# Performance work log

Hardware: AMD Instinct MI355X
Metric: run time of the kernel (lower is better)

The kernel has to match this reference:

```python
import jax, jax.numpy as jnp
import numpy as np

DIM = 2048; H = 16; QLR = 512; KVLR = 512
NOPE = 128; ROPE = 64; VHD = 128
QKHD = NOPE + ROPE
SCALE = QKHD ** -0.5
EPS = 1.1920929e-07  # torch RMSNorm default eps = finfo(float32).eps
B = 1; S = 2048

def _rmsnorm(x, w):
    return x * jax.lax.rsqrt(jnp.mean(x * x, axis=-1, keepdims=True) + EPS) * w

def _rope(x, cos, sin):
    # x: [b, s, h, d]; cos/sin: [s, d//2] (consecutive-pair complex rotation)
    b, s, h, d = x.shape
    x2 = x.reshape(b, s, h, d // 2, 2)
    x0, x1 = x2[..., 0], x2[..., 1]
    c = cos[None, :, None, :]; sn = sin[None, :, None, :]
    y = jnp.stack([x0 * c - x1 * sn, x0 * sn + x1 * c], axis=-1)
    return y.reshape(b, s, h, d)

def setup_inputs() -> dict:
    key = jax.random.key(0)
    ks = jax.random.split(key, 12)
    def lin(k, fan_in, fan_out):
        bound = 1.0 / np.sqrt(fan_in)
        kw, kb = jax.random.split(k)
        w = jax.random.uniform(kw, (fan_out, fan_in), jnp.float32, -bound, bound)
        b = jax.random.uniform(kb, (fan_out,), jnp.float32, -bound, bound)
        return w, b
    x = jax.random.normal(ks[0], (B, S, DIM), jnp.float32)
    theta = jax.random.uniform(ks[1], (S, ROPE // 2), jnp.float32, 0.0, 2 * np.pi)
    freqs_cos = jnp.cos(theta); freqs_sin = jnp.sin(theta)
    mask = jnp.where(jnp.triu(jnp.ones((S, S), bool), k=1), jnp.float32(-1e9), jnp.float32(0.0))
    wq_a_w, wq_a_b = lin(ks[2], DIM, QLR)
    q_norm_w = jnp.ones((QLR,), jnp.float32)
    wq_b_w, wq_b_b = lin(ks[3], QLR, H * QKHD)
    wkv_a_w, wkv_a_b = lin(ks[4], DIM, KVLR + ROPE)
    kv_norm_w = jnp.ones((KVLR,), jnp.float32)
    wkv_b_w, wkv_b_b = lin(ks[5], KVLR, H * (NOPE + VHD))
    wo_w, wo_b = lin(ks[6], H * VHD, DIM)
    return {"x": x, "start_pos": 0, "freqs_cos": freqs_cos, "freqs_sin": freqs_sin,
            "mask": mask, "wq_a_w": wq_a_w, "wq_a_b": wq_a_b, "q_norm_w": q_norm_w,
            "wq_b_w": wq_b_w, "wq_b_b": wq_b_b, "wkv_a_w": wkv_a_w, "wkv_a_b": wkv_a_b,
            "kv_norm_w": kv_norm_w, "wkv_b_w": wkv_b_w, "wkv_b_b": wkv_b_b,
            "wo_w": wo_w, "wo_b": wo_b}

def reference(x, start_pos, freqs_cos, freqs_sin, mask,
              wq_a_w, wq_a_b, q_norm_w, wq_b_w, wq_b_b,
              wkv_a_w, wkv_a_b, kv_norm_w, wkv_b_w, wkv_b_b, wo_w, wo_b):
    bsz, seqlen, _ = x.shape
    # low-rank query: wq_b(q_norm(wq_a(x)))
    q = _rmsnorm(x @ wq_a_w.T + wq_a_b, q_norm_w) @ wq_b_w.T + wq_b_b
    q = q.reshape(bsz, seqlen, H, QKHD)
    q_nope, q_pe = q[..., :NOPE], q[..., NOPE:]
    q_pe = _rope(q_pe, freqs_cos, freqs_sin)
    kv = x @ wkv_a_w.T + wkv_a_b
    kv_lat, k_pe = kv[..., :KVLR], kv[..., KVLR:]
    k_pe = _rope(k_pe[:, :, None, :], freqs_cos, freqs_sin)  # [b,s,1,ROPE]
    q = jnp.concatenate([q_nope, q_pe], axis=-1)
    kvb = (_rmsnorm(kv_lat, kv_norm_w) @ wkv_b_w.T + wkv_b_b).reshape(bsz, seqlen, H, NOPE + VHD)
    k_nope, v = kvb[..., :NOPE], kvb[..., NOPE:]
    k = jnp.concatenate([k_nope, jnp.broadcast_to(k_pe, (bsz, seqlen, H, ROPE))], axis=-1)
    # prefill (start_pos=0): cache[:end_pos] == freshly written k/v
    scores = jnp.einsum('bshd,bthd->bsht', q, k) * SCALE
    scores = scores + mask[None, :, None, :]
    probs = jax.nn.softmax(scores.astype(jnp.float32), axis=-1).astype(x.dtype)
    out = jnp.einsum('bsht,bthd->bshd', probs, v).reshape(bsz, seqlen, H * VHD)
    return out @ wo_w.T + wo_b
```

## Files before the change

### kernel.cpp

```cpp
#include <hip/hip_runtime.h>
#include <hip/hip_bf16.h>

typedef __attribute__((ext_vector_type(8))) short short8x;
typedef __attribute__((ext_vector_type(4))) short short4x;
typedef __attribute__((ext_vector_type(4))) float float4x;
typedef __hip_bfloat16 bf16;

#define EPS_F 1.1920929e-07f
#define SCALE_F 0.07216878364870323f

__device__ inline float rdv(const void* p, size_t i, int f32) {
  return f32 ? ((const float*)p)[i] : __bfloat162float(((const bf16*)p)[i]);
}

__device__ inline int4 pack8(const float* s) {
  unsigned short h[8];
#pragma unroll
  for (int t = 0; t < 8; t++) {
    bf16 b = __float2bfloat16(s[t]);
    __builtin_memcpy(&h[t], &b, 2);
  }
  int4 r;
  r.x = (int)((unsigned)h[0] | ((unsigned)h[1] << 16));
  r.y = (int)((unsigned)h[2] | ((unsigned)h[3] << 16));
  r.z = (int)((unsigned)h[4] | ((unsigned)h[5] << 16));
  r.w = (int)((unsigned)h[6] | ((unsigned)h[7] << 16));
  return r;
}

typedef __attribute__((address_space(1))) const unsigned int gu32;
typedef __attribute__((address_space(3))) unsigned int lu32;
__device__ __forceinline__ void gload16(const void* g, void* l) {
  __builtin_amdgcn_global_load_lds((gu32*)g, (lu32*)l, 16, 0, 0);
}

__device__ __forceinline__ int detect_exponents(const unsigned short* __restrict__ x,
                                                int tid, int* red) {
  int cnt = 0;
#pragma unroll
  for (int i = 0; i < 4; i++) {
    unsigned short u = x[tid * 4 + i];
    int e = (u >> 7) & 0xFF;
    cnt += (e >= 118 && e <= 130) ? 1 : 0;
  }
#pragma unroll
  for (int off = 1; off < 64; off <<= 1) cnt += __shfl_xor(cnt, off);
  if ((tid & 63) == 0) red[tid >> 6] = cnt;
  __syncthreads();
  return ((red[0] + red[1] + red[2] + red[3]) > 768) ? 0 : 1;
}

__global__ __launch_bounds__(256) void detect_dtype(const unsigned short* __restrict__ x,
                                                    int* __restrict__ flag) {
  __shared__ int red[4];
  int f = detect_exponents(x, threadIdx.x, red);
  if (threadIdx.x == 0) flag[0] = f;
}

__global__ __launch_bounds__(256) void sentinel_kernel(bf16* out, int n) {
  int i = blockIdx.x * 256 + threadIdx.x;
  if (i < n) out[i] = __float2bfloat16(1000.0f);
}

__device__ __forceinline__ void cvt8(const void* src, bf16* dst, size_t i, int f32) {
  if (f32) {
    float4 a = *(const float4*)((const float*)src + i);
    float4 b = *(const float4*)((const float*)src + i + 4);
    float s[8] = {a.x, a.y, a.z, a.w, b.x, b.y, b.z, b.w};
    *(int4*)(dst + i) = pack8(s);
  } else {
    *(int4*)(dst + i) = *(const int4*)((const bf16*)src + i);
  }
}

__global__ __launch_bounds__(256) void convert_in1(
    const void* __restrict__ x, const void* __restrict__ wqa,
    const void* __restrict__ wkva,
    const void* __restrict__ qab, const void* __restrict__ kvab,
    bf16* __restrict__ xb, bf16* __restrict__ wqab, bf16* __restrict__ wkvab,
    bf16* __restrict__ qabb, bf16* __restrict__ kvabb,
    const int* __restrict__ flagp)
{
  const int f32 = flagp[0];
  const int b = blockIdx.x, tid = threadIdx.x;
  if (b < 2048)       { size_t i = ((size_t)b * 256 + tid) * 8;          cvt8(x,    xb,    i, f32); }
  else if (b < 2560)  { size_t i = ((size_t)(b - 2048) * 256 + tid) * 8; cvt8(wqa,  wqab,  i, f32); }
  else if (b < 3136)  { size_t i = ((size_t)(b - 2560) * 256 + tid) * 8; cvt8(wkva, wkvab, i, f32); }
  else {
    for (int i = tid; i < 512; i += 256) qabb[i]  = __float2bfloat16(rdv(qab,  i, f32));
    for (int i = tid; i < 576; i += 256) kvabb[i] = __float2bfloat16(rdv(kvab, i, f32));
  }
}

__global__ __launch_bounds__(256) void convert_in2(
    const void* __restrict__ wqb, const void* __restrict__ wkvb,
    const void* __restrict__ qbb, const void* __restrict__ kvbb,
    bf16* __restrict__ wqbb, bf16* __restrict__ wkvbb,
    bf16* __restrict__ qbbb, bf16* __restrict__ kvbbb,
    const int* __restrict__ flagp)
{
  const int f32 = flagp[0];
  const int b = blockIdx.x, tid = threadIdx.x;
  if (b < 768)        { size_t i = ((size_t)b * 256 + tid) * 8;          cvt8(wqb,  wqbb,  i, f32); }
  else if (b < 1792)  { size_t i = ((size_t)(b - 768) * 256 + tid) * 8;  cvt8(wkvb, wkvbb, i, f32); }
  else if (b == 1792) { for (int i = tid; i < 3072; i += 256) qbbb[i]  = __float2bfloat16(rdv(qbb,  i, f32)); }
  else                { for (int i = tid; i < 4096; i += 256) kvbbb[i] = __float2bfloat16(rdv(kvbb, i, f32)); }
}

__global__ __launch_bounds__(256) void convert_wo(
    const void* __restrict__ wo, const void* __restrict__ wob_in,
    bf16* __restrict__ wo16, bf16* __restrict__ wob16,
    const int* __restrict__ flagp)
{
  const int f32 = flagp[0];
  const int b = blockIdx.x, tid = threadIdx.x;
  if (b < 2048) { size_t i = ((size_t)b * 256 + tid) * 8; cvt8(wo, wo16, i, f32); }
  else { for (int i = tid; i < 2048; i += 256) wob16[i] = __float2bfloat16(rdv(wob_in, i, f32)); }
}

__global__ __launch_bounds__(256) void convert_all(
    const void* __restrict__ x,
    const void* __restrict__ wqa, const void* __restrict__ wkva,
    const void* __restrict__ qab, const void* __restrict__ kvab,
    const void* __restrict__ wqb, const void* __restrict__ wkvb,
    const void* __restrict__ qbb, const void* __restrict__ kvbb,
    const void* __restrict__ wo, const void* __restrict__ wob_in,
    bf16* __restrict__ xb, bf16* __restrict__ wqab, bf16* __restrict__ wkvab,
    bf16* __restrict__ qabb, bf16* __restrict__ kvabb,
    bf16* __restrict__ wqbb, bf16* __restrict__ wkvbb,
    bf16* __restrict__ qbbb, bf16* __restrict__ kvbbb,
    bf16* __restrict__ wo16, bf16* __restrict__ wob16,
    int* __restrict__ flag)
{
  __shared__ int red[4];
  const int b = blockIdx.x, tid = threadIdx.x;
  const int f32 = detect_exponents((const unsigned short*)x, tid, red);
  if (b < 2048)       { size_t i = ((size_t)b * 256 + tid) * 8;          cvt8(x,    xb,    i, f32); }
  else if (b < 2560)  { size_t i = ((size_t)(b - 2048) * 256 + tid) * 8; cvt8(wqa,  wqab,  i, f32); }
  else if (b < 3136)  { size_t i = ((size_t)(b - 2560) * 256 + tid) * 8; cvt8(wkva, wkvab, i, f32); }
  else if (b == 3136) {
    for (int i = tid; i < 512; i += 256) qabb[i]  = __float2bfloat16(rdv(qab,  i, f32));
    for (int i = tid; i < 576; i += 256) kvabb[i] = __float2bfloat16(rdv(kvab, i, f32));
    if (tid == 0) flag[0] = f32;
  }
  else if (b < 5185)  { size_t i = ((size_t)(b - 3137) * 256 + tid) * 8; cvt8(wo, wo16, i, f32); }
  else if (b == 5185) { for (int i = tid; i < 2048; i += 256) wob16[i] = __float2bfloat16(rdv(wob_in, i, f32)); }
  else if (b < 5954)  { size_t i = ((size_t)(b - 5186) * 256 + tid) * 8; cvt8(wqb,  wqbb,  i, f32); }
  else if (b < 6978)  { size_t i = ((size_t)(b - 5954) * 256 + tid) * 8; cvt8(wkvb, wkvbb, i, f32); }
  else if (b == 6978) { for (int i = tid; i < 3072; i += 256) qbbb[i]  = __float2bfloat16(rdv(qbb,  i, f32)); }
  else                { for (int i = tid; i < 4096; i += 256) kvbbb[i] = __float2bfloat16(rdv(kvbb, i, f32)); }
}

template<int OMODE, bool A_DYN>
__device__ __forceinline__ void gemm128_body(
    const void* __restrict__ A, const void* __restrict__ W,
    const void* __restrict__ bias, void* __restrict__ Cout,
    int M, int N, int K, int f32in, int bx, int by,
    int kbeg, int kend, int addbias)
{
  __shared__ int4 As4[128 * 4];
  __shared__ int4 Bs4[128 * 4];
  const int tid = threadIdx.x, lane = tid & 63, wave = tid >> 6;
  const int grp = lane >> 4, l16 = lane & 15;
  const int m0 = bx * 128, n0 = by * 128;
  const int wm = (wave & 1) * 64, wn = (wave >> 1) * 64;
  float4x acc[4][4] = {};
  for (int k0 = kbeg; k0 < kend; k0 += 32) {
    if (!f32in) {
#pragma unroll
      for (int j = 0; j < 2; j++) {
        int row = wave * 32 + j * 16 + (lane >> 2);
        int cs = (lane & 3) ^ ((row >> 1) & 3);
        gload16((const bf16*)A + (size_t)(m0 + row) * K + k0 + cs * 8,
                &As4[(wave * 32 + j * 16) * 4]);
        gload16((const bf16*)W + (size_t)(n0 + row) * K + k0 + cs * 8,
                &Bs4[(wave * 32 + j * 16) * 4]);
      }
    } else {
#pragma unroll
      for (int i = 0; i < 2; i++) {
        int ch = tid + i * 256;
        int row = ch >> 2, c = ch & 3;
        int cs = c ^ ((row >> 1) & 3);
        size_t aoff = (size_t)(m0 + row) * K + k0 + cs * 8;
        size_t boff = (size_t)(n0 + row) * K + k0 + cs * 8;
        As4[row * 4 + c] = A_DYN ? pack8((const float*)A + aoff)
                                 : *(const int4*)((const bf16*)A + aoff);
        Bs4[row * 4 + c] = pack8((const float*)W + boff);
      }
    }
    __syncthreads();
    short8x af[4], bfr[4];
#pragma unroll
    for (int i = 0; i < 4; i++) {
      int ra = wm + i * 16 + l16;
      int rb = wn + i * 16 + l16;
      af[i]  = *(const short8x*)&As4[ra * 4 + (grp ^ ((ra >> 1) & 3))];
      bfr[i] = *(const short8x*)&Bs4[rb * 4 + (grp ^ ((rb >> 1) & 3))];
    }
#pragma unroll
    for (int i = 0; i < 4; i++)
#pragma unroll
      for (int j = 0; j < 4; j++)
        acc[i][j] = __builtin_amdgcn_mfma_f32_16x16x32_bf16(af[i], bfr[j], acc[i][j], 0, 0, 0);
    __syncthreads();
  }
#pragma unroll
  for (int j = 0; j < 4; j++) {
    int gn = n0 + wn + j * 16 + l16;
    float bv = addbias ? rdv(bias, gn, f32in) : 0.0f;
#pragma unroll
    for (int i = 0; i < 4; i++) {
      int gm0 = m0 + wm + i * 16 + grp * 4;
#pragma unroll
      for (int r = 0; r < 4; r++) {
        float v = acc[i][j][r] + bv;
        size_t idx = (size_t)(gm0 + r) * N + gn;
        if (OMODE == 0)      ((float*)Cout)[idx] = v;
        else if (OMODE == 1) ((bf16*)Cout)[idx] = __float2bfloat16(v);
        else {
          if (f32in) ((float*)Cout)[idx] = v;
          else       ((bf16*)Cout)[idx] = __float2bfloat16(v);
        }
      }
    }
  }
}

__global__ __launch_bounds__(256) void gemmB_dual(
    const void* __restrict__ A0, const void* __restrict__ A1,
    const void* __restrict__ W0, const void* __restrict__ W1,
    const void* __restrict__ b0, const void* __restrict__ b1,
    void* __restrict__ C0, void* __restrict__ C1)
{
  const int z = blockIdx.z;
  if (z == 0 && blockIdx.y >= 24) return;
  const void* A = z ? A1 : A0;
  const void* W = z ? W1 : W0;
  const void* bias = z ? b1 : b0;
  void* C = z ? C1 : C0;
  const int N = z ? 4096 : 3072;
  gemm128_body<1, false>(A, W, bias, C, 2048, N, 512, 0,
                         blockIdx.x, blockIdx.y, 0, 512, 1);
}

__global__ __launch_bounds__(256) void gemmWo_sk(
    const void* __restrict__ A, const void* __restrict__ W,
    const void* __restrict__ bias, float* __restrict__ part,
    const int* __restrict__ flagp)
{
  const int z = blockIdx.z;
  gemm128_body<0, false>(A, W, bias, part + (size_t)z * 2048 * 2048,
                         2048, 2048, 2048, flagp[0],
                         blockIdx.x, blockIdx.y, z * 1024, z * 1024 + 1024, z == 0);
}

__global__ __launch_bounds__(256) void gemmWo_sk_bf(
    const void* __restrict__ A, const void* __restrict__ W,
    const void* __restrict__ bias, float* __restrict__ part)
{
  const int z = blockIdx.z;
  gemm128_body<0, false>(A, W, bias, part + (size_t)z * 2048 * 2048,
                         2048, 2048, 2048, 0,
                         blockIdx.x, blockIdx.y, z * 1024, z * 1024 + 1024, z == 0);
}

__global__ __launch_bounds__(256) void reduce_out(
    const float* __restrict__ p0, const float* __restrict__ p1,
    void* __restrict__ out, const int* __restrict__ flagp)
{
  const int f32in = flagp[0];
  size_t i = ((size_t)blockIdx.x * 256 + threadIdx.x) * 4;
  float4 a = *(const float4*)(p0 + i);
  float4 b = *(const float4*)(p1 + i);
  a.x += b.x; a.y += b.y; a.z += b.z; a.w += b.w;
  if (f32in) {
    *(float4*)((float*)out + i) = a;
  } else {
    unsigned short h[4];
    bf16 t0 = __float2bfloat16(a.x); __builtin_memcpy(&h[0], &t0, 2);
    bf16 t1 = __float2bfloat16(a.y); __builtin_memcpy(&h[1], &t1, 2);
    bf16 t2 = __float2bfloat16(a.z); __builtin_memcpy(&h[2], &t2, 2);
    bf16 t3 = __float2bfloat16(a.w); __builtin_memcpy(&h[3], &t3, 2);
    int2 v;
    v.x = (int)((unsigned)h[0] | ((unsigned)h[1] << 16));
    v.y = (int)((unsigned)h[2] | ((unsigned)h[3] << 16));
    *(int2*)((bf16*)out + i) = v;
  }
}

template<int OMODE, bool A_DYN>
__device__ __forceinline__ void gemm64_body(
    const void* __restrict__ A, const void* __restrict__ W,
    const void* __restrict__ bias, void* __restrict__ Cout,
    int M, int N, int K, int f32in, int bx, int by,
    int kbeg, int kend, int addbias)
{
  __shared__ int4 As4[64 * 4];
  __shared__ int4 Bs4[64 * 4];
  const int tid = threadIdx.x, lane = tid & 63, wave = tid >> 6;
  const int grp = lane >> 4, l16 = lane & 15;
  const int m0 = bx * 64, n0 = by * 64;
  const int wm = (wave & 1) * 32, wn = (wave >> 1) * 32;
  float4x acc[2][2] = {};
  for (int k0 = kbeg; k0 < kend; k0 += 32) {
    if (!f32in) {
      int row = wave * 16 + (lane >> 2);
      int cs = (lane & 3) ^ ((row >> 1) & 3);
      gload16((const bf16*)A + (size_t)(m0 + row) * K + k0 + cs * 8,
              &As4[wave * 16 * 4]);
      gload16((const bf16*)W + (size_t)(n0 + row) * K + k0 + cs * 8,
              &Bs4[wave * 16 * 4]);
    } else {
      int row = tid >> 2, c = tid & 3;
      int cs = c ^ ((row >> 1) & 3);
      size_t aoff = (size_t)(m0 + row) * K + k0 + cs * 8;
      size_t boff = (size_t)(n0 + row) * K + k0 + cs * 8;
      As4[row * 4 + c] = A_DYN ? pack8((const float*)A + aoff)
                               : *(const int4*)((const bf16*)A + aoff);
      Bs4[row * 4 + c] = pack8((const float*)W + boff);
    }
    __syncthreads();
    short8x af[2], bfr[2];
#pragma unroll
    for (int i = 0; i < 2; i++) {
      int ra = wm + i * 16 + l16;
      int rb = wn + i * 16 + l16;
      af[i]  = *(const short8x*)&As4[ra * 4 + (grp ^ ((ra >> 1) & 3))];
      bfr[i] = *(const short8x*)&Bs4[rb * 4 + (grp ^ ((rb >> 1) & 3))];
    }
#pragma unroll
    for (int i = 0; i < 2; i++)
#pragma unroll
      for (int j = 0; j < 2; j++)
        acc[i][j] = __builtin_amdgcn_mfma_f32_16x16x32_bf16(af[i], bfr[j], acc[i][j], 0, 0, 0);
    __syncthreads();
  }
#pragma unroll
  for (int j = 0; j < 2; j++) {
    int gn = n0 + wn + j * 16 + l16;
    float bv = addbias ? rdv(bias, gn, f32in) : 0.0f;
#pragma unroll
    for (int i = 0; i < 2; i++) {
      int gm0 = m0 + wm + i * 16 + grp * 4;
#pragma unroll
      for (int r = 0; r < 4; r++) {
        float v = acc[i][j][r] + bv;
        size_t idx = (size_t)(gm0 + r) * N + gn;
        if (OMODE == 0)      ((float*)Cout)[idx] = v;
        else if (OMODE == 1) ((bf16*)Cout)[idx] = __float2bfloat16(v);
        else {
          if (f32in) ((float*)Cout)[idx] = v;
          else       ((bf16*)Cout)[idx] = __float2bfloat16(v);
        }
      }
    }
  }
}

__global__ __launch_bounds__(256) void gemmA_sk(
    const void* __restrict__ A,
    const void* __restrict__ W0, const void* __restrict__ W1,
    const void* __restrict__ b0, const void* __restrict__ b1,
    float* __restrict__ C0, float* __restrict__ C1)
{
  const int z = blockIdx.z;
  const int mat = z >> 1, kh = z & 1;
  const int N = mat ? 576 : 512;
  if (blockIdx.y * 64 >= N) return;
  const void* W = mat ? W1 : W0;
  const void* bias = mat ? b1 : b0;
  float* C = (mat ? C1 : C0) + (size_t)kh * 2048 * N;
  gemm64_body<0, false>(A, W, bias, C, 2048, N, 2048, 0,
                        blockIdx.x, blockIdx.y,
                        kh * 1024, kh * 1024 + 1024, kh == 0);
}

__global__ __launch_bounds__(256) void norms_merged(
    const float* __restrict__ q_a0, const float* __restrict__ q_a1,
    const float* __restrict__ kv_a0, const float* __restrict__ kv_a1,
    const void* __restrict__ qw, const void* __restrict__ kvw,
    const void* __restrict__ cosb, const void* __restrict__ sinb,
    bf16* __restrict__ qn, bf16* __restrict__ kvn, bf16* __restrict__ kpe,
    const int* __restrict__ flagp)
{
  const int f32in = flagp[0];
  const int b = blockIdx.x, tid = threadIdx.x;
  __shared__ float red[4];
  if (b < 2048) {
    const int s = b;
    size_t base = (size_t)s * 512;
    float v0 = q_a0[base + tid] + q_a1[base + tid];
    float v1 = q_a0[base + tid + 256] + q_a1[base + tid + 256];
    float ss = v0 * v0 + v1 * v1;
#pragma unroll
    for (int off = 1; off < 64; off <<= 1) ss += __shfl_xor(ss, off);
    if ((tid & 63) == 0) red[tid >> 6] = ss;
    __syncthreads();
    float tot = red[0] + red[1] + red[2] + red[3];
    float scale = rsqrtf(tot * (1.0f / 512.0f) + EPS_F);
    qn[base + tid]       = __float2bfloat16(v0 * scale * rdv(qw, tid, f32in));
    qn[base + tid + 256] = __float2bfloat16(v1 * scale * rdv(qw, tid + 256, f32in));
  } else {
    const int s = b - 2048;
    size_t base = (size_t)s * 576;
    float v0 = kv_a0[base + tid] + kv_a1[base + tid];
    float v1 = kv_a0[base + tid + 256] + kv_a1[base + tid + 256];
    float ss = v0 * v0 + v1 * v1;
#pragma unroll
    for (int off = 1; off < 64; off <<= 1) ss += __shfl_xor(ss, off);
    if ((tid & 63) == 0) red[tid >> 6] = ss;
    __syncthreads();
    float tot = red[0] + red[1] + red[2] + red[3];
    float scale = rsqrtf(tot * (1.0f / 512.0f) + EPS_F);
    kvn[(size_t)s * 512 + tid]       = __float2bfloat16(v0 * scale * rdv(kvw, tid, f32in));
    kvn[(size_t)s * 512 + tid + 256] = __float2bfloat16(v1 * scale * rdv(kvw, tid + 256, f32in));
    if (tid < 32) {
      float x0 = kv_a0[base + 512 + 2 * tid] + kv_a1[base + 512 + 2 * tid];
      float x1 = kv_a0[base + 512 + 2 * tid + 1] + kv_a1[base + 512 + 2 * tid + 1];
      float c  = rdv(cosb, (size_t)s * 32 + tid, f32in);
      float sn = rdv(sinb, (size_t)s * 32 + tid, f32in);
      kpe[s * 64 + 2 * tid]     = __float2bfloat16(x0 * c - x1 * sn);
      kpe[s * 64 + 2 * tid + 1] = __float2bfloat16(x0 * sn + x1 * c);
    }
  }
}

__global__ __launch_bounds__(256) void rope_vt_merged(
    bf16* __restrict__ q, const void* __restrict__ cosb,
    const void* __restrict__ sinb, const bf16* __restrict__ kvb,
    bf16* __restrict__ Vt, const int* __restrict__ flagp)
{
  const int b = blockIdx.x, tid = threadIdx.x;
  __shared__ __align__(16) bf16 tile[64][136];
  if (b < 2048) {
    const int f32in = flagp[0];
    const int s = b;
#pragma unroll
    for (int it = 0; it < 2; it++) {
      int p = tid + it * 256;
      int hh = p >> 5, jj = p & 31;
      bf16* src = q + (size_t)s * 3072 + hh * 192 + 128 + 2 * jj;
      float x0 = __bfloat162float(src[0]);
      float x1 = __bfloat162float(src[1]);
      float c  = rdv(cosb, (size_t)s * 32 + jj, f32in);
      float sn = rdv(sinb, (size_t)s * 32 + jj, f32in);
      src[0] = __float2bfloat16(x0 * c - x1 * sn);
      src[1] = __float2bfloat16(x0 * sn + x1 * c);
    }
  } else {
    const int hb = b - 2048;
    const int h = hb & 15;
    const int t0 = (hb >> 4) * 64;
#pragma unroll
    for (int i = 0; i < 4; i++) {
      int chunk = tid + i * 256;
      int row = chunk >> 4;
      int c8 = (chunk & 15) * 8;
      *(int4*)&tile[row][c8] =
          *(const int4*)(kvb + (size_t)(t0 + row) * 4096 + h * 256 + 128 + c8);
    }
    __syncthreads();
#pragma unroll
    for (int i = 0; i < 32; i++) {
      int idx = tid + i * 256;
      int d = idx >> 6;
      int t = idx & 63;
      Vt[((size_t)h * 128 + d) * 2048 + t0 + t] = tile[t][d];
    }
  }
}

__global__ __launch_bounds__(256) void attn_kernel(
    const bf16* __restrict__ Q, const bf16* __restrict__ kvb,
    const bf16* __restrict__ kpe, const bf16* __restrict__ Vt,
    bf16* __restrict__ Out)
{
  __shared__ __align__(16) bf16 Ks[64 * 200];
  __shared__ __align__(16) bf16 Vs[128 * 72];
  __shared__ __align__(16) bf16 plds[4][16 * 68];
  const int b = blockIdx.x;
  const int h = b & 15;
  const int tt = (b >> 4) & 15;
  const int q0 = ((b >> 8) ? (31 - tt) : tt) * 64;
  const int tid = threadIdx.x;
  const int wave = tid >> 6;
  const int lane = tid & 63;
  const int grp = lane >> 4, l16 = lane & 15;
  const int qrt = q0 + wave * 16;
  const bf16* Qbase = Q + (size_t)(qrt + l16) * 3072 + h * 192;
  short8x qf[6];
#pragma unroll
  for (int c = 0; c < 6; c++)
    qf[c] = *(const short8x*)(Qbase + c * 32 + grp * 8);
  float m_run[4], l_run[4];
  float4x o_acc[8] = {};
#pragma unroll
  for (int r = 0; r < 4; r++) { m_run[r] = -__builtin_inff(); l_run[r] = 0.f; }
  bf16* pl = &plds[wave][0];
  for (int t0 = 0; t0 <= q0; t0 += 64) {
#pragma unroll
    for (int i = 0; i < 4; i++) {
      int ch = tid + i * 256;
      int row = ch >> 4, c = ch & 15;
      *(int4*)&Ks[row * 200 + c * 8] =
          *(const int4*)(kvb + (size_t)(t0 + row) * 4096 + h * 256 + c * 8);
    }
#pragma unroll
    for (int i = 0; i < 2; i++) {
      int ch = tid + i * 256;
      int row = ch >> 3, c = ch & 7;
      *(int4*)&Ks[row * 200 + 128 + c * 8] =
          *(const int4*)(kpe + (size_t)(t0 + row) * 64 + c * 8);
    }
#pragma unroll
    for (int i = 0; i < 4; i++) {
      int ch = tid + i * 256;
      int row = ch >> 3, c = ch & 7;
      *(int4*)&Vs[row * 72 + c * 8] =
          *(const int4*)(Vt + ((size_t)h * 128 + row) * 2048 + t0 + c * 8);
    }
    __syncthreads();
    float4x sacc[4] = {};
#pragma unroll
    for (int n = 0; n < 4; n++) {
      const bf16* Kb = &Ks[(n * 16 + l16) * 200 + grp * 8];
#pragma unroll
      for (int c = 0; c < 6; c++) {
        short8x kf = *(const short8x*)(Kb + c * 32);
        sacc[n] = __builtin_amdgcn_mfma_f32_16x16x32_bf16(qf[c], kf, sacc[n], 0, 0, 0);
      }
    }
    float pv[4][4], alpha[4];
#pragma unroll
    for (int r = 0; r < 4; r++) {
      const int s_row = qrt + grp * 4 + r;
      float p0[4];
      float mx = -__builtin_inff();
#pragma unroll
      for (int n = 0; n < 4; n++) {
        int t = t0 + n * 16 + l16;
        float v = sacc[n][r] * SCALE_F;
        v = (t > s_row) ? -1.0e9f : v;
        p0[n] = v;
        mx = fmaxf(mx, v);
      }
      mx = fmaxf(mx, __shfl_xor(mx, 1));
      mx = fmaxf(mx, __shfl_xor(mx, 2));
      mx = fmaxf(mx, __shfl_xor(mx, 4));
      mx = fmaxf(mx, __shfl_xor(mx, 8));
      float m_new = fmaxf(m_run[r], mx);
      float a = __expf(m_run[r] - m_new);
      m_run[r] = m_new;
      float sum = 0.f;
#pragma unroll
      for (int n = 0; n < 4; n++) {
        float e = __expf(p0[n] - m_new);
        pv[n][r] = e;
        sum += e;
      }
      sum += __shfl_xor(sum, 1);
      sum += __shfl_xor(sum, 2);
      sum += __shfl_xor(sum, 4);
      sum += __shfl_xor(sum, 8);
      l_run[r] = l_run[r] * a + sum;
      alpha[r] = a;
    }
#pragma unroll
    for (int n = 0; n < 8; n++)
#pragma unroll
      for (int r = 0; r < 4; r++)
        o_acc[n][r] *= alpha[r];
#pragma unroll
    for (int n = 0; n < 4; n++)
#pragma unroll
      for (int r = 0; r < 4; r++)
        pl[(grp * 4 + r) * 68 + n * 16 + l16] = __float2bfloat16(pv[n][r]);
#pragma unroll
    for (int c = 0; c < 2; c++) {
      union { short4x h4[2]; short8x v8; } pk;
      const bf16* pp = pl + l16 * 68 + c * 32 + grp * 8;
      pk.h4[0] = *(const short4x*)(pp);
      pk.h4[1] = *(const short4x*)(pp + 4);
#pragma unroll
      for (int n = 0; n < 8; n++) {
        short8x vf = *(const short8x*)&Vs[(size_t)(n * 16 + l16) * 72 + c * 32 + grp * 8];
        o_acc[n] = __builtin_amdgcn_mfma_f32_16x16x32_bf16(pk.v8, vf, o_acc[n], 0, 0, 0);
      }
    }
    __syncthreads();
  }
  float inv[4];
#pragma unroll
  for (int r = 0; r < 4; r++) inv[r] = 1.0f / l_run[r];
#pragma unroll
  for (int n = 0; n < 8; n++)
#pragma unroll
    for (int r = 0; r < 4; r++) {
      int s_row = qrt + grp * 4 + r;
      Out[(size_t)s_row * 2048 + h * 128 + n * 16 + l16] =
          __float2bfloat16(o_acc[n][r] * inv[r]);
    }
}

extern "C" void kernel_launch(void* const* d_in, const int* in_sizes, int n_in,
                              void* d_out, int out_size, void* d_ws, size_t ws_size,
                              hipStream_t stream) {
  const void* x        = d_in[0];
  const void* fcos     = d_in[2];
  const void* fsin     = d_in[3];
  const void* wq_a_w   = d_in[5];
  const void* wq_a_b   = d_in[6];
  const void* q_norm_w = d_in[7];
  const void* wq_b_w   = d_in[8];
  const void* wq_b_b   = d_in[9];
  const void* wkv_a_w  = d_in[10];
  const void* wkv_a_b  = d_in[11];
  const void* kv_norm_w= d_in[12];
  const void* wkv_b_w  = d_in[13];
  const void* wkv_b_b  = d_in[14];
  const void* wo_w     = d_in[15];
  const void* wo_b     = d_in[16];

  const size_t KB = 1024, MB = 1024 * 1024;
  if (ws_size < 46 * MB) {
    sentinel_kernel<<<(out_size + 255) / 256, 256, 0, stream>>>((bf16*)d_out, out_size);
    return;
  }
  char* ws = (char*)d_ws;
  bf16*  kpe    = (bf16*)(ws);
  int*   flag   = (int*)(ws + 256 * KB);
  bf16*  qbuf   = (bf16*)(ws + 512 * KB);
  bf16*  kvb    = (bf16*)(ws + 12 * MB + 512 * KB);
  bf16*  Vt     = (bf16*)(ws + 28 * MB + 512 * KB);
  bf16*  attnout= (bf16*)(ws + 36 * MB + 512 * KB);
  float* kv_a0  = (float*)(ws + 512 * KB);
  float* kv_a1  = (float*)(ws + 5 * MB);
  float* q_a0   = (float*)(ws + 36 * MB + 512 * KB);
  float* q_a1   = (float*)(ws + 40 * MB + 512 * KB);
  bf16*  qn     = (bf16*)(ws + 28 * MB + 512 * KB);
  bf16*  kvn    = (bf16*)(ws + 30 * MB + 512 * KB);
  float* wpart  = (float*)(ws + 512 * KB);
  bf16*  xb     = (bf16*)(ws + 12 * MB + 512 * KB);
  bf16*  wqab   = (bf16*)(ws + 20 * MB + 512 * KB);
  bf16*  wkvab  = (bf16*)(ws + 22 * MB + 512 * KB);
  bf16*  qabb   = (bf16*)(ws + 25 * MB);
  bf16*  kvabb  = (bf16*)(ws + 25 * MB + 64 * KB);
  bf16*  wqbb_m = (bf16*)(ws + 36 * MB + 512 * KB);
  bf16*  wkvbb_m= (bf16*)(ws + 39 * MB + 512 * KB);
  bf16*  qbbb_m = (bf16*)(ws + 43 * MB + 512 * KB);
  bf16*  kvbbb_m= (bf16*)(ws + 43 * MB + 768 * KB);
  bf16*  wo16   = (bf16*)(ws + 46 * MB);
  bf16*  wob16  = (bf16*)(ws + 54 * MB + 512 * KB);
  bf16*  wqbb_b = (bf16*)(ws + 56 * MB);
  bf16*  wkvbb_b= (bf16*)(ws + 59 * MB);
  bf16*  qbbb_b = (bf16*)(ws + 63 * MB);
  bf16*  kvbbb_b= (bf16*)(ws + 63 * MB + 64 * KB);

  const bool wofast = (ws_size >= 56 * MB);
  const bool bigws  = (ws_size >= 64 * MB);

  dim3 blk(256);
  if (bigws) {
    convert_all<<<6980, blk, 0, stream>>>(
        x, wq_a_w, wkv_a_w, wq_a_b, wkv_a_b, wq_b_w, wkv_b_w, wq_b_b, wkv_b_b,
        wo_w, wo_b,
        xb, wqab, wkvab, qabb, kvabb, wqbb_b, wkvbb_b, qbbb_b, kvbbb_b,
        wo16, wob16, flag);
    gemmA_sk<<<dim3(32, 9, 4), blk, 0, stream>>>(
        xb, wqab, wkvab, qabb, kvabb, q_a0, kv_a0);
    norms_merged<<<4096, blk, 0, stream>>>(
        q_a0, q_a1, kv_a0, kv_a1, q_norm_w, kv_norm_w, fcos, fsin,
        qn, kvn, kpe, flag);
    gemmB_dual<<<dim3(16, 32, 2), blk, 0, stream>>>(
        qn, kvn, wqbb_b, wkvbb_b, qbbb_b, kvbbb_b, qbuf, kvb);
    rope_vt_merged<<<2560, blk, 0, stream>>>(qbuf, fcos, fsin, kvb, Vt, flag);
    attn_kernel<<<dim3(512), blk, 0, stream>>>(qbuf, kvb, kpe, Vt, attnout);
    gemmWo_sk_bf<<<dim3(16, 16, 2), blk, 0, stream>>>(attnout, wo16, wob16, wpart);
    reduce_out<<<4096, blk, 0, stream>>>(wpart, wpart + (size_t)2048 * 2048, d_out, flag);
  } else {
    detect_dtype<<<1, blk, 0, stream>>>((const unsigned short*)x, flag);
    convert_in1<<<3137, blk, 0, stream>>>(
        x, wq_a_w, wkv_a_w, wq_a_b, wkv_a_b, xb, wqab, wkvab, qabb, kvabb, flag);
    if (wofast)
      convert_wo<<<2049, blk, 0, stream>>>(wo_w, wo_b, wo16, wob16, flag);
    gemmA_sk<<<dim3(32, 9, 4), blk, 0, stream>>>(
        xb, wqab, wkvab, qabb, kvabb, q_a0, kv_a0);
    norms_merged<<<4096, blk, 0, stream>>>(
        q_a0, q_a1, kv_a0, kv_a1, q_norm_w, kv_norm_w, fcos, fsin,
        qn, kvn, kpe, flag);
    convert_in2<<<1794, blk, 0, stream>>>(
        wq_b_w, wkv_b_w, wq_b_b, wkv_b_b, wqbb_m, wkvbb_m, qbbb_m, kvbbb_m, flag);
    gemmB_dual<<<dim3(16, 32, 2), blk, 0, stream>>>(
        qn, kvn, wqbb_m, wkvbb_m, qbbb_m, kvbbb_m, qbuf, kvb);
    rope_vt_merged<<<2560, blk, 0, stream>>>(qbuf, fcos, fsin, kvb, Vt, flag);
    attn_kernel<<<dim3(512), blk, 0, stream>>>(qbuf, kvb, kpe, Vt, attnout);
    if (wofast)
      gemmWo_sk_bf<<<dim3(16, 16, 2), blk, 0, stream>>>(attnout, wo16, wob16, wpart);
    else
      gemmWo_sk<<<dim3(16, 16, 2), blk, 0, stream>>>(attnout, wo_w, wo_b, wpart, flag);
    reduce_out<<<4096, blk, 0, stream>>>(wpart, wpart + (size_t)2048 * 2048, d_out, flag);
  }
}
```

Baseline: 315.3 us.

## Fuse q RoPE and V transpose into the second-stage projection GEMM epilogue

Adds a gemmB_fused kernel that applies rotary embedding to the q_pe columns and writes V in transposed layout straight from the GEMM accumulators. This removes the separate rope_vt_merged pass and its extra global read/write of qbuf and kvb. It is gated on the workspace being at least 68 MB and uses new qn4/kvn4 buffers. The epilogue adds cross-lane shuffles, per-element cos/sin loads and scattered stores, and the K loop loads tiles without double buffering.

```diff
diff --git a/kernel.cpp b/kernel.cpp
--- a/kernel.cpp
+++ b/kernel.cpp
@@ -242,6 +242,120 @@
   const int N = z ? 4096 : 3072;
   gemm128_body<1, false>(A, W, bias, C, 2048, N, 512, 0,
                          blockIdx.x, blockIdx.y, 0, 512, 1);
+}
+
+__global__ __launch_bounds__(256) void gemmB_fused(
+    const bf16* __restrict__ qn, const bf16* __restrict__ kvn,
+    const bf16* __restrict__ Wq, const bf16* __restrict__ Wkv,
+    const bf16* __restrict__ bq, const bf16* __restrict__ bkv,
+    const void* __restrict__ cosb, const void* __restrict__ sinb,
+    bf16* __restrict__ qbuf, bf16* __restrict__ kvb, bf16* __restrict__ Vt,
+    const int* __restrict__ flagp)
+{
+  const int z = blockIdx.z;
+  if (z == 0 && blockIdx.y >= 24) return;
+  const bf16* A = z ? kvn : qn;
+  const bf16* W = z ? Wkv : Wq;
+  const bf16* bias = z ? bkv : bq;
+  const int N = z ? 4096 : 3072;
+  const int K = 512;
+  __shared__ int4 As4[128 * 4];
+  __shared__ int4 Bs4[128 * 4];
+  const int tid = threadIdx.x, lane = tid & 63, wave = tid >> 6;
+  const int grp = lane >> 4, l16 = lane & 15;
+  const int m0 = blockIdx.x * 128, n0 = blockIdx.y * 128;
+  const int wm = (wave & 1) * 64, wn = (wave >> 1) * 64;
+  float4x acc[4][4] = {};
+  for (int k0 = 0; k0 < K; k0 += 32) {
+#pragma unroll
+    for (int j = 0; j < 2; j++) {
+      int row = wave * 32 + j * 16 + (lane >> 2);
+      int cs = (lane & 3) ^ ((row >> 1) & 3);
+      gload16(A + (size_t)(m0 + row) * K + k0 + cs * 8,
+              &As4[(wave * 32 + j * 16) * 4]);
+      gload16(W + (size_t)(n0 + row) * K + k0 + cs * 8,
+              &Bs4[(wave * 32 + j * 16) * 4]);
+    }
+    __syncthreads();
+    short8x af[4], bfr[4];
+#pragma unroll
+    for (int i = 0; i < 4; i++) {
+      int ra = wm + i * 16 + l16;
+      int rb = wn + i * 16 + l16;
+      af[i]  = *(const short8x*)&As4[ra * 4 + (grp ^ ((ra >> 1) & 3))];
+      bfr[i] = *(const short8x*)&Bs4[rb * 4 + (grp ^ ((rb >> 1) & 3))];
+    }
+#pragma unroll
+    for (int i = 0; i < 4; i++)
+#pragma unroll
+      for (int j = 0; j < 4; j++)
+        acc[i][j] = __builtin_amdgcn_mfma_f32_16x16x32_bf16(af[i], bfr[j], acc[i][j], 0, 0, 0);
+    __syncthreads();
+  }
+  const int f32 = flagp[0];
+#pragma unroll
+  for (int j = 0; j < 4; j++) {
+    int gn = n0 + wn + j * 16 + l16;
+    float bv = __bfloat162float(bias[gn]);
+    if (z == 0) {
+      int c12 = (gn >> 4) % 12;
+      if (c12 >= 8) {
+        int jj = ((gn % 192) - 128) >> 1;
+#pragma unroll
+        for (int i = 0; i < 4; i++) {
+          int gm0 = m0 + wm + i * 16 + grp * 4;
+#pragma unroll
+          for (int r = 0; r < 4; r++) {
+            float v = acc[i][j][r] + bv;
+            int s = gm0 + r;
+            float c  = rdv(cosb, (size_t)s * 32 + jj, f32);
+            float sn = rdv(sinb, (size_t)s * 32 + jj, f32);
+            float o = __shfl_xor(v, 1);
+            float res = (l16 & 1) ? (o * sn + v * c)
+                                  : (v * c - o * sn);
+            qbuf[(size_t)s * 3072 + gn] = __float2bfloat16(res);
+          }
+        }
+      } else {
+#pragma unroll
+        for (int i = 0; i < 4; i++) {
+          int gm0 = m0 + wm + i * 16 + grp * 4;
+#pragma unroll
+          for (int r = 0; r < 4; r++)
+            qbuf[(size_t)(gm0 + r) * 3072 + gn] = __float2bfloat16(acc[i][j][r] + bv);
+        }
+      }
+    } else {
+      int c16 = (gn >> 4) & 15;
+      if (c16 >= 8) {
+        int hh = gn >> 8;
+        int d  = (gn & 255) - 128;
+        bf16* vtb = Vt + ((size_t)hh * 128 + d) * 2048;
+#pragma unroll
+        for (int i = 0; i < 4; i++) {
+          int gm0 = m0 + wm + i * 16 + grp * 4;
+          unsigned short hv[4];
+#pragma unroll
+          for (int r = 0; r < 4; r++) {
+            bf16 t = __float2bfloat16(acc[i][j][r] + bv);
+            __builtin_memcpy(&hv[r], &t, 2);
+          }
+          int2 w;
+          w.x = (int)((unsigned)hv[0] | ((unsigned)hv[1] << 16));
+          w.y = (int)((unsigned)hv[2] | ((unsigned)hv[3] << 16));
+          *(int2*)(vtb + gm0) = w;
+        }
+      } else {
+#pragma unroll
+        for (int i = 0; i < 4; i++) {
+          int gm0 = m0 + wm + i * 16 + grp * 4;
+#pragma unroll
+          for (int r = 0; r < 4; r++)
+            kvb[(size_t)(gm0 + r) * 4096 + gn] = __float2bfloat16(acc[i][j][r] + bv);
+        }
+      }
+    }
+  }
 }
 
 __global__ __launch_bounds__(256) void gemmWo_sk(
@@ -656,9 +770,12 @@
   bf16*  wkvbb_b= (bf16*)(ws + 59 * MB);
   bf16*  qbbb_b = (bf16*)(ws + 63 * MB);
   bf16*  kvbbb_b= (bf16*)(ws + 63 * MB + 64 * KB);
+  bf16*  qn4    = (bf16*)(ws + 64 * MB);
+  bf16*  kvn4   = (bf16*)(ws + 66 * MB);
 
   const bool wofast = (ws_size >= 56 * MB);
   const bool bigws  = (ws_size >= 64 * MB);
+  const bool fuseB  = (ws_size >= 68 * MB);
 
   dim3 blk(256);
   if (bigws) {
@@ -669,12 +786,21 @@
         wo16, wob16, flag);
     gemmA_sk<<<dim3(32, 9, 4), blk, 0, stream>>>(
         xb, wqab, wkvab, qabb, kvabb, q_a0, kv_a0);
-    norms_merged<<<4096, blk, 0, stream>>>(
-        q_a0, q_a1, kv_a0, kv_a1, q_norm_w, kv_norm_w, fcos, fsin,
-        qn, kvn, kpe, flag);
-    gemmB_dual<<<dim3(16, 32, 2), blk, 0, stream>>>(
-        qn, kvn, wqbb_b, wkvbb_b, qbbb_b, kvbbb_b, qbuf, kvb);
-    rope_vt_merged<<<2560, blk, 0, stream>>>(qbuf, fcos, fsin, kvb, Vt, flag);
+    if (fuseB) {
+      norms_merged<<<4096, blk, 0, stream>>>(
+          q_a0, q_a1, kv_a0, kv_a1, q_norm_w, kv_norm_w, fcos, fsin,
+          qn4, kvn4, kpe, flag);
+      gemmB_fused<<<dim3(16, 32, 2), blk, 0, stream>>>(
+          qn4, kvn4, wqbb_b, wkvbb_b, qbbb_b, kvbbb_b, fcos, fsin,
+          qbuf, kvb, Vt, flag);
+    } else {
+      norms_merged<<<4096, blk, 0, stream>>>(
+          q_a0, q_a1, kv_a0, kv_a1, q_norm_w, kv_norm_w, fcos, fsin,
+          qn, kvn, kpe, flag);
+      gemmB_dual<<<dim3(16, 32, 2), blk, 0, stream>>>(
+          qn, kvn, wqbb_b, wkvbb_b, qbbb_b, kvbbb_b, qbuf, kvb);
+      rope_vt_merged<<<2560, blk, 0, stream>>>(qbuf, fcos, fsin, kvb, Vt, flag);
+    }
     attn_kernel<<<dim3(512), blk, 0, stream>>>(qbuf, kvb, kpe, Vt, attnout);
     gemmWo_sk_bf<<<dim3(16, 16, 2), blk, 0, stream>>>(attnout, wo16, wob16, wpart);
     reduce_out<<<4096, blk, 0, stream>>>(wpart, wpart + (size_t)2048 * 2048, d_out, flag);
```

Result: no change. 317.9 us (+0.8%).
